# Optimization experiments

Hardware: AMD Instinct MI355X
Metric: run time of the kernel (lower is better)

## Reference

```python
import jax, jax.numpy as jnp
import numpy as np
import math

_EPS = 1e-5          # _SAMPLING_EPS
_K_PER_CHUNK = 32    # _TOPK_K_PER_CHUNK
_MAX_CHUNK = 32768   # _TOPK_MAX_CHUNK_SIZE
B, V = 128, 128256


def setup_inputs() -> dict:
    key = jax.random.key(0)
    ks = jax.random.split(key, 10)
    logits = jax.random.normal(ks[0], (B, V), dtype=jnp.float32) * 4.0
    temperature = jax.random.uniform(ks[1], (B,), dtype=jnp.float32) * 1.5
    top_k = jax.random.randint(ks[2], (B,), 0, 100)  # 0 => top-k disabled
    top_p = 0.5 + 0.5 * jax.random.uniform(ks[3], (B,), dtype=jnp.float32)
    output_token_counts = jax.random.randint(ks[4], (B, V), 0, 3).astype(jnp.float32)
    prompt_token_mask = jax.random.randint(ks[5], (B, V), 0, 2).astype(bool)
    presence_penalties = jax.random.uniform(ks[6], (B,), dtype=jnp.float32)
    frequency_penalties = jax.random.uniform(ks[7], (B,), dtype=jnp.float32)
    repetition_penalties = 1.0 + 0.5 * jax.random.uniform(ks[8], (B,), dtype=jnp.float32)
    u = jax.random.uniform(ks[9], (B, V), dtype=jnp.float32, minval=1e-6, maxval=1.0)
    q_samples = -jnp.log(u)  # Exponential(1) noise, vLLM random_sample convention
    return dict(logits=logits, temperature=temperature, top_k=top_k, top_p=top_p,
                output_token_counts=output_token_counts, prompt_token_mask=prompt_token_mask,
                presence_penalties=presence_penalties, frequency_penalties=frequency_penalties,
                repetition_penalties=repetition_penalties, q_samples=q_samples)


def _apply_penalties(logits, counts, prompt_mask, presence, frequency, repetition):
    counts = counts.astype(logits.dtype)
    prompt_f = prompt_mask.astype(logits.dtype)
    occurred = counts - jnp.maximum(counts - 1.0, 0.0)            # 1 if count>0 else 0
    rep_union = occurred + prompt_f
    rep_mask = rep_union - jnp.maximum(rep_union - 1.0, 0.0)      # 1 if in prompt or output
    rep = repetition[:, None]
    pos = jnp.maximum(logits, 0.0)
    neg = jnp.minimum(logits, 0.0)
    penalized = pos / rep + neg * rep
    logits = logits + rep_mask * (penalized - logits)
    logits = logits - frequency[:, None] * counts - presence[:, None] * occurred
    return logits


def _chunked_topk(logits):
    # split vocab into <=32768 chunks, top-32 per chunk (multi-core ttnn.topk emulation)
    b, v = logits.shape
    num_chunks = math.ceil(v / _MAX_CHUNK)
    chunk_size = math.ceil(v / num_chunks)
    pad = num_chunks * chunk_size - v
    x = jnp.pad(logits, ((0, 0), (0, pad)), constant_values=-np.inf) if pad else logits
    x = x.reshape(b, num_chunks, chunk_size)
    vals, inds = jax.lax.top_k(x, _K_PER_CHUNK)                   # [b, nc, k]
    inds = inds + (jnp.arange(num_chunks, dtype=inds.dtype) * chunk_size)[None, :, None]
    return vals.reshape(b, -1), inds.reshape(b, -1)               # [b, nc*k]


def _filter_topk_topp(all_values, k, p, vocab_size):
    C = all_values.shape[-1]
    probs = jax.nn.softmax(all_values, axis=-1)
    probs_sort = jnp.sort(probs, axis=-1)                         # ascending
    # top-k on candidate set
    count_k = jnp.clip(C - k.astype(jnp.int32), 0, C - 1)[:, None]
    cutoff_k = jnp.take_along_axis(probs_sort, count_k, axis=-1)
    no_k = ((k <= 0) | (k >= vocab_size))[:, None]
    cutoff_k = jnp.where(no_k, -np.inf, cutoff_k)
    all_values = jnp.where(probs < cutoff_k, -np.inf, all_values)
    # top-p on candidate set
    cumprob = jnp.cumsum(probs_sort, axis=-1)
    mask = cumprob <= (1.0 - p)[:, None]
    mask = mask.at[:, -1].set(False)
    count_p = jnp.sum(mask, axis=-1, dtype=jnp.int32)[:, None]
    cutoff_p = jnp.take_along_axis(probs_sort, count_p, axis=-1)
    all_values = jnp.where(probs < cutoff_p, -np.inf, all_values)
    return all_values


def reference(logits, temperature, top_k, top_p, output_token_counts, prompt_token_mask,
              presence_penalties, frequency_penalties, repetition_penalties, q_samples):
    logits = logits.astype(jnp.float32)
    logits = _apply_penalties(logits, output_token_counts, prompt_token_mask,
                              presence_penalties, frequency_penalties, repetition_penalties)
    greedy = jnp.argmax(logits, axis=-1)                          # [B]
    temp_eff = jnp.where(temperature < _EPS, 1.0, temperature)
    logits_t = logits / temp_eff[:, None]
    vals, inds = _chunked_topk(logits_t)                          # [B, 128] each
    filtered = _filter_topk_topp(vals, top_k, top_p, logits.shape[-1])
    probs = jax.nn.softmax(filtered, axis=-1)                     # fp32 softmax on candidates
    q_red = jnp.take_along_axis(q_samples, inds, axis=1)
    local = jnp.argmax(probs / q_red, axis=-1)                    # exponential-noise sampling
    random_sampled = jnp.take_along_axis(inds, local[:, None], axis=1)[:, 0]
    sampled = jnp.where(temperature < _EPS, greedy, random_sampled.astype(greedy.dtype))
    return sampled[:, None], probs                                # sampled_token_ids [B,1]
```

## Files before the change

### kernel.cpp

```cpp
#include <hip/hip_runtime.h>
#include <math.h>

#define BATCH   128
#define VOCAB   128256
#define NCHUNK  4
#define CSIZE   32064
#define CVEC    (CSIZE / 4)
#define T1      256
#define NBKT    2048
#define CAP     2048
#define KSEL    32
#define CWIDTH  (NCHUNK * KSEL)
#define T2      128

__device__ __forceinline__ unsigned fenc(float f) {
    unsigned u = __float_as_uint(f);
    return (u & 0x80000000u) ? ~u : (u | 0x80000000u);
}

__device__ __forceinline__ float penalize(float l, float cnt, float pf,
                                          float rep, float freq, float pres) {
    float occ   = __fsub_rn(cnt, fmaxf(__fsub_rn(cnt, 1.0f), 0.0f));
    float ru    = __fadd_rn(occ, pf);
    float rmask = __fsub_rn(ru, fmaxf(__fsub_rn(ru, 1.0f), 0.0f));
    float pos   = fmaxf(l, 0.0f);
    float neg   = fminf(l, 0.0f);
    float pen   = __fadd_rn(__fdiv_rn(pos, rep), __fmul_rn(neg, rep));
    float p     = __fadd_rn(l, __fmul_rn(rmask, __fsub_rn(pen, l)));
    p = __fsub_rn(p, __fmul_rn(freq, cnt));
    p = __fsub_rn(p, __fmul_rn(pres, occ));
    return p;
}

__global__ void detect_mask_kernel(const unsigned* __restrict__ w, int* __restrict__ flag) {
    __shared__ int s_all01, s_allf;
    if (threadIdx.x == 0) { s_all01 = 1; s_allf = 1; }
    __syncthreads();
    int all01 = 1, allf = 1;
    for (int i = threadIdx.x; i < 4096; i += blockDim.x) {
        unsigned x = w[i];
        if (!(x == 0u || x == 1u)) all01 = 0;
        if (!(x == 0u || x == 0x3F800000u)) allf = 0;
    }
    if (!all01) atomicAnd(&s_all01, 0);
    if (!allf)  atomicAnd(&s_allf, 0);
    __syncthreads();
    if (threadIdx.x == 0) *flag = s_all01 ? 1 : (s_allf ? 2 : 0);
}

__device__ __forceinline__ void load_pf(const void* pmask, long base, int i,
                                        int mtype, float pfv[4]) {
    if (mtype == 1) {
        int4 mi = ((const int4*)((const int*)pmask + base))[i];
        pfv[0] = mi.x ? 1.0f : 0.0f; pfv[1] = mi.y ? 1.0f : 0.0f;
        pfv[2] = mi.z ? 1.0f : 0.0f; pfv[3] = mi.w ? 1.0f : 0.0f;
    } else if (mtype == 2) {
        float4 mf = ((const float4*)((const float*)pmask + base))[i];
        pfv[0] = mf.x; pfv[1] = mf.y; pfv[2] = mf.z; pfv[3] = mf.w;
    } else {
        unsigned mm = ((const unsigned*)((const unsigned char*)pmask + base))[i];
        pfv[0] = (mm & 0x000000ffu) ? 1.0f : 0.0f;
        pfv[1] = (mm & 0x0000ff00u) ? 1.0f : 0.0f;
        pfv[2] = (mm & 0x00ff0000u) ? 1.0f : 0.0f;
        pfv[3] = (mm & 0xff000000u) ? 1.0f : 0.0f;
    }
}

__global__ __launch_bounds__(T1) void sampler_k1(
    const float* __restrict__ logits, const float* __restrict__ counts,
    const void* __restrict__ pmask, const int* __restrict__ mflag,
    const float* __restrict__ temperature, const float* __restrict__ presence,
    const float* __restrict__ frequency, const float* __restrict__ repetition,
    float* __restrict__ g_topv, int* __restrict__ g_topi,
    float* __restrict__ g_gval, int* __restrict__ g_gidx)
{
    const int b   = blockIdx.x >> 2;
    const int c   = blockIdx.x & 3;
    const int tid = threadIdx.x;
    const long base = (long)b * VOCAB + (long)c * CSIZE;
    const int mtype = *mflag;

    __shared__ unsigned hist[NBKT];
    __shared__ float    cv[CAP];
    __shared__ int      ci[CAP];
    __shared__ unsigned ccnt;
    __shared__ int      s_tb;
    __shared__ float    rv[T1];
    __shared__ int      rix[T1];

    for (int i = tid; i < NBKT; i += T1) hist[i] = 0;
    if (tid == 0) ccnt = 0;

    const float temp = temperature[b];
    const float teff = (temp < 1e-5f) ? 1.0f : temp;
    const float pres = presence[b];
    const float freq = frequency[b];
    const float rep  = repetition[b];

    float gmax = -INFINITY;
    int   gidx = 0x7fffffff;

    __syncthreads();

    const float4* l4 = (const float4*)(logits + base);
    const float4* c4 = (const float4*)(counts + base);

    for (int i = tid; i < CVEC; i += T1) {
        float4 lv = l4[i];
        float4 cc = c4[i];
        float pfv[4];
        load_pf(pmask, base, i, mtype, pfv);
        float le[4] = {lv.x, lv.y, lv.z, lv.w};
        float ce[4] = {cc.x, cc.y, cc.z, cc.w};
#pragma unroll
        for (int e = 0; e < 4; ++e) {
            float p = penalize(le[e], ce[e], pfv[e], rep, freq, pres);
            int idx = i * 4 + e;
            if (p > gmax) { gmax = p; gidx = idx; }
            float v = __fdiv_rn(p, teff);
            atomicAdd(&hist[fenc(v) >> 21], 1u);
        }
    }

    rv[tid] = gmax; rix[tid] = gidx;
    __syncthreads();
    for (int s = T1 / 2; s > 0; s >>= 1) {
        if (tid < s) {
            float ov = rv[tid + s]; int oi = rix[tid + s];
            if (ov > rv[tid] || (ov == rv[tid] && oi < rix[tid])) { rv[tid] = ov; rix[tid] = oi; }
        }
        __syncthreads();
    }
    if (tid == 0) {
        g_gval[blockIdx.x] = rv[0];
        g_gidx[blockIdx.x] = c * CSIZE + rix[0];
        unsigned acc = 0; int tb = 0;
        for (int q = NBKT - 1; q >= 0; --q) {
            acc += hist[q];
            if (acc >= KSEL) { tb = q; break; }
        }
        s_tb = tb;
    }
    __syncthreads();
    const unsigned thr = ((unsigned)s_tb) << 21;

    for (int i = tid; i < CVEC; i += T1) {
        float4 lv = l4[i];
        float4 cc = c4[i];
        float pfv[4];
        load_pf(pmask, base, i, mtype, pfv);
        float le[4] = {lv.x, lv.y, lv.z, lv.w};
        float ce[4] = {cc.x, cc.y, cc.z, cc.w};
#pragma unroll
        for (int e = 0; e < 4; ++e) {
            float p = penalize(le[e], ce[e], pfv[e], rep, freq, pres);
            float v = __fdiv_rn(p, teff);
            if (fenc(v) >= thr) {
                unsigned pos = atomicAdd(&ccnt, 1u);
                if (pos < CAP) { cv[pos] = v; ci[pos] = i * 4 + e; }
            }
        }
    }
    __syncthreads();

    unsigned m = ccnt;
    if (m > CAP) m = CAP;
    unsigned P = KSEL;
    while (P < m) P <<= 1;
    for (unsigned s = m + tid; s < P; s += T1) { cv[s] = -INFINITY; ci[s] = 0x7fffffff; }
    __syncthreads();

    for (unsigned k = 2; k <= P; k <<= 1) {
        for (unsigned j = k >> 1; j > 0; j >>= 1) {
            for (unsigned s = tid; s < P; s += T1) {
                unsigned x = s ^ j;
                if (x > s) {
                    float av = cv[s], bv = cv[x];
                    int   ai = ci[s], bi = ci[x];
                    bool xBetter = (bv > av) || (bv == av && bi < ai);
                    bool sBetter = (av > bv) || (av == bv && ai < bi);
                    bool doSwap  = ((s & k) == 0) ? xBetter : sBetter;
                    if (doSwap) { cv[s] = bv; cv[x] = av; ci[s] = bi; ci[x] = ai; }
                }
            }
            __syncthreads();
        }
    }

    if (tid < KSEL) {
        int o = blockIdx.x * KSEL + tid;
        g_topv[o] = cv[tid];
        g_topi[o] = c * CSIZE + ci[tid];
    }
}

__global__ __launch_bounds__(T2) void sampler_k2(
    const float* __restrict__ g_topv, const int* __restrict__ g_topi,
    const float* __restrict__ g_gval, const int* __restrict__ g_gidx,
    const float* __restrict__ temperature, const int* __restrict__ topk,
    const float* __restrict__ topp, const float* __restrict__ qs,
    float* __restrict__ out)
{
    const int b = blockIdx.x;
    const int j = threadIdx.x;

    __shared__ int   ix[T2];
    __shared__ float sv[T2];
    __shared__ float cum[T2];
    __shared__ float red[T2];
    __shared__ int   redi[T2];

    float val = g_topv[b * CWIDTH + j];
    int   idx = g_topi[b * CWIDTH + j];
    ix[j] = idx;

    red[j] = val; __syncthreads();
    for (int s = T2 / 2; s > 0; s >>= 1) {
        if (j < s) red[j] = fmaxf(red[j], red[j + s]);
        __syncthreads();
    }
    float m1 = red[0]; __syncthreads();
    float e = expf(__fsub_rn(val, m1));
    red[j] = e; __syncthreads();
    for (int s = T2 / 2; s > 0; s >>= 1) {
        if (j < s) red[j] = __fadd_rn(red[j], red[j + s]);
        __syncthreads();
    }
    float s1 = red[0]; __syncthreads();
    float prob = __fdiv_rn(e, s1);
    sv[j] = prob;
    __syncthreads();

    for (unsigned k = 2; k <= (unsigned)T2; k <<= 1) {
        for (unsigned jj = k >> 1; jj > 0; jj >>= 1) {
            unsigned x = (unsigned)j ^ jj;
            if (x > (unsigned)j) {
                float a = sv[j], bb = sv[x];
                bool sw = (((unsigned)j & k) == 0) ? (a > bb) : (a < bb);
                if (sw) { sv[j] = bb; sv[x] = a; }
            }
            __syncthreads();
        }
    }

    if (j == 0) {
        float a = 0.0f;
        for (int t = 0; t < T2; ++t) { a = __fadd_rn(a, sv[t]); cum[t] = a; }
    }
    __syncthreads();

    const int   k_row = topk[b];
    const float p_row = topp[b];
    int count_k = CWIDTH - k_row;
    count_k = min(max(count_k, 0), CWIDTH - 1);
    float cutoff_k = sv[count_k];
    if (k_row <= 0 || k_row >= VOCAB) cutoff_k = -INFINITY;

    float lim = __fsub_rn(1.0f, p_row);
    bool mk = (j < CWIDTH - 1) && (cum[j] <= lim);
    redi[j] = mk ? 1 : 0; __syncthreads();
    for (int s = T2 / 2; s > 0; s >>= 1) {
        if (j < s) redi[j] += redi[j + s];
        __syncthreads();
    }
    int count_p = redi[0]; __syncthreads();
    float cutoff_p = sv[count_p];

    float f = val;
    if (prob < cutoff_k) f = -INFINITY;
    if (prob < cutoff_p) f = -INFINITY;

    red[j] = f; __syncthreads();
    for (int s = T2 / 2; s > 0; s >>= 1) {
        if (j < s) red[j] = fmaxf(red[j], red[j + s]);
        __syncthreads();
    }
    float m2 = red[0]; __syncthreads();
    float e2 = (f == -INFINITY) ? 0.0f : expf(__fsub_rn(f, m2));
    red[j] = e2; __syncthreads();
    for (int s = T2 / 2; s > 0; s >>= 1) {
        if (j < s) red[j] = __fadd_rn(red[j], red[j + s]);
        __syncthreads();
    }
    float s2 = red[0]; __syncthreads();
    float pf = __fdiv_rn(e2, s2);
    out[BATCH + b * CWIDTH + j] = pf;

    float q = qs[(long)b * VOCAB + idx];
    float ratio = __fdiv_rn(pf, q);
    red[j] = ratio; redi[j] = j;
    __syncthreads();
    for (int s = T2 / 2; s > 0; s >>= 1) {
        if (j < s) {
            float o = red[j + s]; int oi = redi[j + s];
            if (o > red[j] || (o == red[j] && oi < redi[j])) { red[j] = o; redi[j] = oi; }
        }
        __syncthreads();
    }

    if (j == 0) {
        float bvv = g_gval[b * NCHUNK]; int bii = g_gidx[b * NCHUNK];
        for (int c2 = 1; c2 < NCHUNK; ++c2) {
            float w = g_gval[b * NCHUNK + c2]; int wi = g_gidx[b * NCHUNK + c2];
            if (w > bvv || (w == bvv && wi < bii)) { bvv = w; bii = wi; }
        }
        int token = ix[redi[0]];
        float tmp = temperature[b];
        int samp = (tmp < 1e-5f) ? bii : token;
        out[b] = (float)samp;
    }
}

extern "C" void kernel_launch(void* const* d_in, const int* in_sizes, int n_in,
                              void* d_out, int out_size, void* d_ws, size_t ws_size,
                              hipStream_t stream) {
    const float* logits = (const float*)d_in[0];
    const float* temp   = (const float*)d_in[1];
    const int*   topk   = (const int*)d_in[2];
    const float* topp   = (const float*)d_in[3];
    const float* counts = (const float*)d_in[4];
    const void*  pmask  = d_in[5];
    const float* pres   = (const float*)d_in[6];
    const float* freq   = (const float*)d_in[7];
    const float* rep    = (const float*)d_in[8];
    const float* qs     = (const float*)d_in[9];
    float* out = (float*)d_out;

    int*   mflag  = (int*)d_ws;
    float* wsf    = (float*)((char*)d_ws + 64);
    float* g_topv = wsf;
    int*   g_topi = (int*)(g_topv + BATCH * CWIDTH);
    float* g_gval = (float*)(g_topi + BATCH * CWIDTH);
    int*   g_gidx = (int*)(g_gval + BATCH * NCHUNK);

    detect_mask_kernel<<<1, 256, 0, stream>>>((const unsigned*)pmask, mflag);

    sampler_k1<<<BATCH * NCHUNK, T1, 0, stream>>>(
        logits, counts, pmask, mflag, temp, pres, freq, rep,
        g_topv, g_topi, g_gval, g_gidx);

    sampler_k2<<<BATCH, T2, 0, stream>>>(
        g_topv, g_topi, g_gval, g_gidx, temp, topk, topp, qs, out);
}
```

Baseline: 338.9 us.

## Fold mask detection into main kernel, widen blocks, use wave-shuffle reductions

Removes the separate mask-type detection launch by having every k1 block redundantly scan the first 4096 words of the mask into shared flags. Raises the k1 block size from 256 to 1024 threads so the 512 blocks have more threads each streaming the chunk. Replaces the shared-memory tree argmax with wavefront shuffles plus a 16-entry cross-wave pass, and replaces the serial 2048-bucket threshold scan with a 64-lane parallel suffix scan. The trade-off is extra redundant mask reads per block and higher contention on the shared histogram atomics.

```diff
diff --git a/kernel.cpp b/kernel.cpp
--- a/kernel.cpp
+++ b/kernel.cpp
@@ -6,7 +6,7 @@
 #define NCHUNK  4
 #define CSIZE   32064
 #define CVEC    (CSIZE / 4)
-#define T1      256
+#define T1      1024
 #define NBKT    2048
 #define CAP     2048
 #define KSEL    32
@@ -30,22 +30,6 @@
     p = __fsub_rn(p, __fmul_rn(freq, cnt));
     p = __fsub_rn(p, __fmul_rn(pres, occ));
     return p;
-}
-
-__global__ void detect_mask_kernel(const unsigned* __restrict__ w, int* __restrict__ flag) {
-    __shared__ int s_all01, s_allf;
-    if (threadIdx.x == 0) { s_all01 = 1; s_allf = 1; }
-    __syncthreads();
-    int all01 = 1, allf = 1;
-    for (int i = threadIdx.x; i < 4096; i += blockDim.x) {
-        unsigned x = w[i];
-        if (!(x == 0u || x == 1u)) all01 = 0;
-        if (!(x == 0u || x == 0x3F800000u)) allf = 0;
-    }
-    if (!all01) atomicAnd(&s_all01, 0);
-    if (!allf)  atomicAnd(&s_allf, 0);
-    __syncthreads();
-    if (threadIdx.x == 0) *flag = s_all01 ? 1 : (s_allf ? 2 : 0);
 }
 
 __device__ __forceinline__ void load_pf(const void* pmask, long base, int i,
@@ -68,7 +52,7 @@
 
 __global__ __launch_bounds__(T1) void sampler_k1(
     const float* __restrict__ logits, const float* __restrict__ counts,
-    const void* __restrict__ pmask, const int* __restrict__ mflag,
+    const void* __restrict__ pmask,
     const float* __restrict__ temperature, const float* __restrict__ presence,
     const float* __restrict__ frequency, const float* __restrict__ repetition,
     float* __restrict__ g_topv, int* __restrict__ g_topi,
@@ -78,18 +62,33 @@
     const int c   = blockIdx.x & 3;
     const int tid = threadIdx.x;
     const long base = (long)b * VOCAB + (long)c * CSIZE;
-    const int mtype = *mflag;
 
     __shared__ unsigned hist[NBKT];
     __shared__ float    cv[CAP];
     __shared__ int      ci[CAP];
     __shared__ unsigned ccnt;
     __shared__ int      s_tb;
-    __shared__ float    rv[T1];
-    __shared__ int      rix[T1];
+    __shared__ int      s_m0, s_mf;
+    __shared__ float    wrv[16];
+    __shared__ int      wri[16];
 
     for (int i = tid; i < NBKT; i += T1) hist[i] = 0;
-    if (tid == 0) ccnt = 0;
+    if (tid == 0) { ccnt = 0; s_m0 = 1; s_mf = 1; }
+    __syncthreads();
+
+    {
+        const unsigned* w = (const unsigned*)pmask;
+        int a01 = 1, af = 1;
+        for (int i = tid; i < 4096; i += T1) {
+            unsigned x = w[i];
+            if (!(x == 0u || x == 1u)) a01 = 0;
+            if (!(x == 0u || x == 0x3F800000u)) af = 0;
+        }
+        if (!a01) atomicAnd(&s_m0, 0);
+        if (!af)  atomicAnd(&s_mf, 0);
+    }
+    __syncthreads();
+    const int mtype = s_m0 ? 1 : (s_mf ? 2 : 0);
 
     const float temp = temperature[b];
     const float teff = (temp < 1e-5f) ? 1.0f : temp;
@@ -97,13 +96,11 @@
     const float freq = frequency[b];
     const float rep  = repetition[b];
 
+    const float4* l4 = (const float4*)(logits + base);
+    const float4* c4 = (const float4*)(counts + base);
+
     float gmax = -INFINITY;
     int   gidx = 0x7fffffff;
-
-    __syncthreads();
-
-    const float4* l4 = (const float4*)(logits + base);
-    const float4* c4 = (const float4*)(counts + base);
 
     for (int i = tid; i < CVEC; i += T1) {
         float4 lv = l4[i];
@@ -122,24 +119,43 @@
         }
     }
 
-    rv[tid] = gmax; rix[tid] = gidx;
-    __syncthreads();
-    for (int s = T1 / 2; s > 0; s >>= 1) {
-        if (tid < s) {
-            float ov = rv[tid + s]; int oi = rix[tid + s];
-            if (ov > rv[tid] || (ov == rv[tid] && oi < rix[tid])) { rv[tid] = ov; rix[tid] = oi; }
-        }
-        __syncthreads();
-    }
+    for (int off = 32; off > 0; off >>= 1) {
+        float ov = __shfl_down(gmax, off);
+        int   oi = __shfl_down(gidx, off);
+        if (ov > gmax || (ov == gmax && oi < gidx)) { gmax = ov; gidx = oi; }
+    }
+    if ((tid & 63) == 0) { wrv[tid >> 6] = gmax; wri[tid >> 6] = gidx; }
+    __syncthreads();
     if (tid == 0) {
-        g_gval[blockIdx.x] = rv[0];
-        g_gidx[blockIdx.x] = c * CSIZE + rix[0];
-        unsigned acc = 0; int tb = 0;
-        for (int q = NBKT - 1; q >= 0; --q) {
-            acc += hist[q];
-            if (acc >= KSEL) { tb = q; break; }
-        }
-        s_tb = tb;
+        float bv = wrv[0]; int bi = wri[0];
+        for (int w2 = 1; w2 < 16; ++w2) {
+            if (wrv[w2] > bv || (wrv[w2] == bv && wri[w2] < bi)) { bv = wrv[w2]; bi = wri[w2]; }
+        }
+        g_gval[blockIdx.x] = bv;
+        g_gidx[blockIdx.x] = c * CSIZE + bi;
+    }
+
+    if (tid < 64) {
+        const int gb = tid * 32;
+        unsigned gs = 0;
+#pragma unroll
+        for (int k = 0; k < 32; ++k) gs += hist[gb + k];
+        unsigned suf = gs;
+#pragma unroll
+        for (int off = 1; off < 64; off <<= 1) {
+            unsigned o = __shfl_down(suf, off);
+            if (tid + off < 64) suf += o;
+        }
+        unsigned sufn = __shfl_down(suf, 1);
+        if (tid == 63) sufn = 0;
+        if (suf >= (unsigned)KSEL && sufn < (unsigned)KSEL) {
+            unsigned acc = sufn; int tb = gb;
+            for (int q = gb + 31; q >= gb; --q) {
+                acc += hist[q];
+                if (acc >= (unsigned)KSEL) { tb = q; break; }
+            }
+            s_tb = tb;
+        }
     }
     __syncthreads();
     const unsigned thr = ((unsigned)s_tb) << 21;
@@ -326,17 +342,13 @@
     const float* qs     = (const float*)d_in[9];
     float* out = (float*)d_out;
 
-    int*   mflag  = (int*)d_ws;
-    float* wsf    = (float*)((char*)d_ws + 64);
-    float* g_topv = wsf;
+    float* g_topv = (float*)d_ws;
     int*   g_topi = (int*)(g_topv + BATCH * CWIDTH);
     float* g_gval = (float*)(g_topi + BATCH * CWIDTH);
     int*   g_gidx = (int*)(g_gval + BATCH * NCHUNK);
 
-    detect_mask_kernel<<<1, 256, 0, stream>>>((const unsigned*)pmask, mflag);
-
     sampler_k1<<<BATCH * NCHUNK, T1, 0, stream>>>(
-        logits, counts, pmask, mflag, temp, pres, freq, rep,
+        logits, counts, pmask, temp, pres, freq, rep,
         g_topv, g_topi, g_gval, g_gidx);
 
     sampler_k2<<<BATCH, T2, 0, stream>>>(
```

After: 295.1 us. 1.15x faster.
